# Performance work log

Measured on AMD Instinct MI355X. Metric: run time of the kernel, lower is better.

Reference implementation:

```python
import jax, jax.numpy as jnp
import numpy as np

N, D, H = 32768, 512, 8
HD = D // H  # head_dim = 64
LN_EPS = 1e-5


def setup_inputs() -> dict:
    key = jax.random.key(0)
    ks = jax.random.split(key, 5)
    s = 1.0 / np.sqrt(D)
    return {
        "h": jax.random.normal(ks[0], (N, D), dtype=jnp.float32),
        "Wq": jax.random.normal(ks[1], (D, D), dtype=jnp.float32) * s,
        "Wk": jax.random.normal(ks[2], (D, D), dtype=jnp.float32) * s,
        "Wv": jax.random.normal(ks[3], (D, D), dtype=jnp.float32) * s,
        "Wf": jax.random.normal(ks[4], (D, D), dtype=jnp.float32) * s,
        "ln_gamma": jnp.ones((D,), dtype=jnp.float32),
        "ln_beta": jnp.zeros((D,), dtype=jnp.float32),
    }


def _layernorm(x, g, b):
    mu = jnp.mean(x, axis=-1, keepdims=True)
    var = jnp.mean(jnp.square(x - mu), axis=-1, keepdims=True)
    return (x - mu) * jax.lax.rsqrt(var + LN_EPS) * g + b


def reference(h, Wq, Wk, Wv, Wf, ln_gamma, ln_beta):
    n = h.shape[0]
    # projections (torch Linear y = x @ W^T; weights here stored as [in,out])
    q = jax.nn.relu((h @ Wq).reshape(n, H, HD))
    k = jax.nn.relu((h @ Wk).reshape(n, H, HD))
    v = (h @ Wv).reshape(n, H, HD)
    # per-node outer-product accumulation over heads (n = head axis here)
    kv = jnp.einsum('bnd,bne->bde', k, v)          # [N, HD, HD]
    num = jnp.einsum('bnd,bde->bne', q, kv)        # [N, H, HD]
    denom = jnp.einsum('bnd,bd->bn', q, k.sum(axis=1))  # [N, H]
    attn = num / denom[..., None]                  # [N, H, HD]
    fh = attn.reshape(n, D) @ Wf                   # dropout = identity (eval)
    out = _layernorm(h + fh, ln_gamma, ln_beta)
    return (out, q, k, v)
```

## Files before the change

### kernel.cpp

```cpp
#include <hip/hip_runtime.h>
#include <hip/hip_bf16.h>

#define NROWS 32768
#define DIM   512
#define HEADS 8
#define LN_EPS 1e-5f

typedef __attribute__((ext_vector_type(8))) short short8;
typedef __attribute__((ext_vector_type(4))) float floatx4;

typedef __attribute__((address_space(3))) void lds_void;
typedef __attribute__((address_space(1))) void gbl_void;

__device__ __forceinline__ void async16(const void* g, void* l) {
    __builtin_amdgcn_global_load_lds(
        (gbl_void*)(unsigned long long)(uintptr_t)g,
        (lds_void*)(unsigned int)(uintptr_t)l,
        16, 0, 0);
}

__global__ __launch_bounds__(256) void hconv_kernel(
    const float* __restrict__ h, __hip_bfloat16* __restrict__ hb)
{
    const size_t i = ((size_t)blockIdx.x * 256 + threadIdx.x) * 4;
    const float4 f = *(const float4*)(h + i);
    union { ushort4 u; __hip_bfloat16 b[4]; } pk;
    pk.b[0] = __float2bfloat16(f.x);
    pk.b[1] = __float2bfloat16(f.y);
    pk.b[2] = __float2bfloat16(f.z);
    pk.b[3] = __float2bfloat16(f.w);
    *(ushort4*)(hb + i) = pk.u;
}

__global__ __launch_bounds__(256) void wtrans_kernel(
    const float* __restrict__ Wq, const float* __restrict__ Wk,
    const float* __restrict__ Wv, const float* __restrict__ Wf,
    __hip_bfloat16* __restrict__ Wt)
{
    __shared__ float tile[32][33];
    const int z = blockIdx.z;
    const float* W = (z == 0) ? Wq : (z == 1) ? Wk : (z == 2) ? Wv : Wf;
    __hip_bfloat16* dst = Wt + (size_t)z * DIM * DIM;

    const int bn = blockIdx.x * 32;
    const int bk = blockIdx.y * 32;
    const int tx = threadIdx.x & 31;
    const int ty = threadIdx.x >> 5;
    #pragma unroll
    for (int i = ty; i < 32; i += 8)
        tile[i][tx] = W[(size_t)(bk + i) * DIM + bn + tx];
    __syncthreads();
    #pragma unroll
    for (int i = ty; i < 32; i += 8)
        dst[(size_t)(bn + i) * DIM + bk + tx] = __float2bfloat16(tile[tx][i]);
}

__global__ __launch_bounds__(256) void mfma_gemm_kernel(
    const __hip_bfloat16* __restrict__ A,
    const __hip_bfloat16* __restrict__ Bt,
    float* __restrict__ C, int qkv)
{
    __shared__ __align__(16) char smem[32768];

    const int t    = threadIdx.x;
    const int lane = t & 63;
    const int w    = t >> 6;
    const int wm   = w >> 1, wn = w & 1;
    const int l16  = lane & 15, quad = lane >> 4;

    const int nwg  = gridDim.x * gridDim.y;
    int flat = blockIdx.y * gridDim.x + blockIdx.x;
    flat = (flat & 7) * (nwg >> 3) + (flat >> 3);
    const int bx = flat % gridDim.x;
    const int by = flat / gridDim.x;

    const int bm = by * 128;
    const int bn = bx * 128;

    float* Cp;
    int ccol, relu;
    if (qkv) {
        Cp   = C + (size_t)(bx >> 2) * ((size_t)NROWS * DIM);
        ccol = (bx & 3) * 128;
        relu = (bx >> 2) < 2;
    } else {
        Cp = C; ccol = bn; relu = 0;
    }

    const int c0 = w * 128 + lane;
    const int c1 = c0 + 64;
    const int r0 = c0 >> 2, kq0 = (c0 & 3) ^ ((r0 >> 1) & 3);
    const int r1 = c1 >> 2, kq1 = (c1 & 3) ^ ((r1 >> 1) & 3);

    const int offA0 = (bm + r0) * DIM + kq0 * 8;
    const int offA1 = (bm + r1) * DIM + kq1 * 8;
    const int offB0 = (bn + r0) * DIM + kq0 * 8;
    const int offB1 = (bn + r1) * DIM + kq1 * 8;
    const int ldsC0 = (w * 128) * 16;
    const int ldsC1 = (w * 128 + 64) * 16;

    int aoff[4], boff[4];
    #pragma unroll
    for (int i = 0; i < 4; ++i) {
        const int ra = wm * 64 + i * 16 + l16;
        aoff[i] = (ra * 4 + (quad ^ ((ra >> 1) & 3))) * 16;
        const int rb = wn * 64 + i * 16 + l16;
        boff[i] = 8192 + (rb * 4 + (quad ^ ((rb >> 1) & 3))) * 16;
    }

    floatx4 acc[4][4];
    #pragma unroll
    for (int i = 0; i < 4; ++i)
        #pragma unroll
        for (int j = 0; j < 4; ++j)
            acc[i][j] = (floatx4){0.f, 0.f, 0.f, 0.f};

    #define STAGE(tt) do {                                                  \
        char* _b = smem + ((tt) & 1) * 16384;                               \
        const int _k0 = (tt) * 32;                                          \
        async16(A  + offA0 + _k0, _b + ldsC0);                              \
        async16(A  + offA1 + _k0, _b + ldsC1);                              \
        async16(Bt + offB0 + _k0, _b + 8192 + ldsC0);                       \
        async16(Bt + offB1 + _k0, _b + 8192 + ldsC1);                       \
    } while (0)

    #define COMPUTE(tt) do {                                                \
        const char* _b = smem + ((tt) & 1) * 16384;                         \
        short8 af[4], bf[4];                                                \
        _Pragma("unroll")                                                   \
        for (int i = 0; i < 4; ++i) af[i] = *(const short8*)(_b + aoff[i]); \
        _Pragma("unroll")                                                   \
        for (int j = 0; j < 4; ++j) bf[j] = *(const short8*)(_b + boff[j]); \
        _Pragma("unroll")                                                   \
        for (int i = 0; i < 4; ++i)                                         \
            _Pragma("unroll")                                               \
            for (int j = 0; j < 4; ++j)                                     \
                acc[i][j] = __builtin_amdgcn_mfma_f32_16x16x32_bf16(        \
                    af[i], bf[j], acc[i][j], 0, 0, 0);                      \
    } while (0)

    STAGE(0);
    for (int kt = 0; kt < 15; ++kt) {
        STAGE(kt + 1);
        asm volatile("s_waitcnt vmcnt(4)\n\ts_barrier" ::: "memory");
        COMPUTE(kt);
        asm volatile("s_barrier" ::: "memory");
    }
    asm volatile("s_waitcnt vmcnt(0)\n\ts_barrier" ::: "memory");
    COMPUTE(15);

    #undef STAGE
    #undef COMPUTE

    #pragma unroll
    for (int i = 0; i < 4; ++i) {
        const int gr = bm + wm * 64 + i * 16 + quad * 4;
        #pragma unroll
        for (int j = 0; j < 4; ++j) {
            const int gc = ccol + wn * 64 + j * 16 + l16;
            #pragma unroll
            for (int rg = 0; rg < 4; ++rg) {
                float vv = acc[i][j][rg];
                if (relu) vv = fmaxf(vv, 0.f);
                Cp[(size_t)(gr + rg) * DIM + gc] = vv;
            }
        }
    }
}

__global__ __launch_bounds__(256) void attn_kernel(
    const float* __restrict__ q, const float* __restrict__ k,
    const float* __restrict__ v, __hip_bfloat16* __restrict__ attn)
{
    __shared__ float sq[4][8][68];
    __shared__ float sk[4][8][68];
    __shared__ float sv[4][8][68];

    const int t = threadIdx.x;
    const int w = t >> 6, lane = t & 63;
    const size_t base = ((size_t)blockIdx.x * 4 + w) * DIM;

    const int sh = lane >> 3;
    const int sd = (lane & 7) * 8;
    {
        const float4 q0 = ((const float4*)(q + base))[lane * 2];
        const float4 q1 = ((const float4*)(q + base))[lane * 2 + 1];
        const float4 k0 = ((const float4*)(k + base))[lane * 2];
        const float4 k1 = ((const float4*)(k + base))[lane * 2 + 1];
        const float4 v0 = ((const float4*)(v + base))[lane * 2];
        const float4 v1 = ((const float4*)(v + base))[lane * 2 + 1];
        *(float4*)&sq[w][sh][sd]     = q0;
        *(float4*)&sq[w][sh][sd + 4] = q1;
        *(float4*)&sk[w][sh][sd]     = k0;
        *(float4*)&sk[w][sh][sd + 4] = k1;
        *(float4*)&sv[w][sh][sd]     = v0;
        *(float4*)&sv[w][sh][sd + 4] = v1;
    }
    __syncthreads();

    const int n  = lane >> 3;
    const int hh = lane & 7;
    float s = 0.f;
    #pragma unroll
    for (int d = 0; d < 64; d += 4) {
        const float4 a = *(const float4*)&sq[w][n][d];
        const float4 b = *(const float4*)&sk[w][hh][d];
        s += a.x * b.x + a.y * b.y + a.z * b.z + a.w * b.w;
    }
    float den = s;
    den += __shfl_xor(den, 1);
    den += __shfl_xor(den, 2);
    den += __shfl_xor(den, 4);
    const float p = s / den;

    float pl[8];
    #pragma unroll
    for (int h = 0; h < 8; ++h) pl[h] = __shfl(p, (lane & 56) | h);

    const int eg = (lane & 7) * 8;
    float o[8] = {0.f, 0.f, 0.f, 0.f, 0.f, 0.f, 0.f, 0.f};
    #pragma unroll
    for (int h = 0; h < 8; ++h) {
        const float4 v0 = *(const float4*)&sv[w][h][eg];
        const float4 v1 = *(const float4*)&sv[w][h][eg + 4];
        o[0] += pl[h] * v0.x; o[1] += pl[h] * v0.y;
        o[2] += pl[h] * v0.z; o[3] += pl[h] * v0.w;
        o[4] += pl[h] * v1.x; o[5] += pl[h] * v1.y;
        o[6] += pl[h] * v1.z; o[7] += pl[h] * v1.w;
    }
    union { short8 s8; __hip_bfloat16 b[8]; } pk;
    #pragma unroll
    for (int j = 0; j < 8; ++j) pk.b[j] = __float2bfloat16(o[j]);
    *(short8*)(attn + base + (size_t)lane * 8) = pk.s8;
}

__global__ __launch_bounds__(256) void ln_kernel(
    const float* __restrict__ h, const float* fh,
    const float* __restrict__ gamma, const float* __restrict__ beta,
    float* out)
{
    const int lane = threadIdx.x & 63;
    const int wave = threadIdx.x >> 6;
    const size_t base = ((size_t)blockIdx.x * 4 + wave) * DIM;

    const float4 a0 = ((const float4*)(h + base))[lane * 2];
    const float4 a1 = ((const float4*)(h + base))[lane * 2 + 1];
    const float4 b0 = ((const float4*)(fh + base))[lane * 2];
    const float4 b1 = ((const float4*)(fh + base))[lane * 2 + 1];

    float x[8];
    x[0] = a0.x + b0.x; x[1] = a0.y + b0.y; x[2] = a0.z + b0.z; x[3] = a0.w + b0.w;
    x[4] = a1.x + b1.x; x[5] = a1.y + b1.y; x[6] = a1.z + b1.z; x[7] = a1.w + b1.w;

    float s = 0.f;
    #pragma unroll
    for (int i = 0; i < 8; ++i) s += x[i];
    #pragma unroll
    for (int off = 32; off > 0; off >>= 1) s += __shfl_down(s, off);
    const float mu = __shfl(s, 0) * (1.f / DIM);

    float vs = 0.f;
    #pragma unroll
    for (int i = 0; i < 8; ++i) { const float d = x[i] - mu; vs += d * d; }
    #pragma unroll
    for (int off = 32; off > 0; off >>= 1) vs += __shfl_down(vs, off);
    const float rstd = rsqrtf(__shfl(vs, 0) * (1.f / DIM) + LN_EPS);

    const float4 g0 = ((const float4*)gamma)[lane * 2];
    const float4 g1 = ((const float4*)gamma)[lane * 2 + 1];
    const float4 e0 = ((const float4*)beta)[lane * 2];
    const float4 e1 = ((const float4*)beta)[lane * 2 + 1];

    float4 r0, r1;
    r0.x = (x[0] - mu) * rstd * g0.x + e0.x;
    r0.y = (x[1] - mu) * rstd * g0.y + e0.y;
    r0.z = (x[2] - mu) * rstd * g0.z + e0.z;
    r0.w = (x[3] - mu) * rstd * g0.w + e0.w;
    r1.x = (x[4] - mu) * rstd * g1.x + e1.x;
    r1.y = (x[5] - mu) * rstd * g1.y + e1.y;
    r1.z = (x[6] - mu) * rstd * g1.z + e1.z;
    r1.w = (x[7] - mu) * rstd * g1.w + e1.w;

    ((float4*)(out + base))[lane * 2]     = r0;
    ((float4*)(out + base))[lane * 2 + 1] = r1;
}

extern "C" void kernel_launch(void* const* d_in, const int* in_sizes, int n_in,
                              void* d_out, int out_size, void* d_ws, size_t ws_size,
                              hipStream_t stream)
{
    const float* h     = (const float*)d_in[0];
    const float* Wq    = (const float*)d_in[1];
    const float* Wk    = (const float*)d_in[2];
    const float* Wv    = (const float*)d_in[3];
    const float* Wf    = (const float*)d_in[4];
    const float* gamma = (const float*)d_in[5];
    const float* beta  = (const float*)d_in[6];

    const size_t ND = (size_t)NROWS * DIM;
    float* out = (float*)d_out;
    float* qo  = out + ND;
    float* ko  = out + 2 * ND;
    float* vo  = out + 3 * ND;
    float* fh  = out;

    __hip_bfloat16* hb  = (__hip_bfloat16*)d_ws;
    __hip_bfloat16* wt  = hb + ND;
    __hip_bfloat16* wtf = wt + 3 * DIM * DIM;
    __hip_bfloat16* attnb = hb;

    hconv_kernel<<<NROWS * DIM / 1024, 256, 0, stream>>>(h, hb);
    wtrans_kernel<<<dim3(16, 16, 4), 256, 0, stream>>>(Wq, Wk, Wv, Wf, wt);

    mfma_gemm_kernel<<<dim3(12, NROWS / 128), 256, 0, stream>>>(hb, wt, qo, 1);

    attn_kernel<<<NROWS / 4, 256, 0, stream>>>(qo, ko, vo, attnb);

    mfma_gemm_kernel<<<dim3(4, NROWS / 128), 256, 0, stream>>>(attnb, wtf, fh, 0);

    ln_kernel<<<NROWS / 4, 256, 0, stream>>>(h, fh, gamma, beta, out);
}
```

Baseline: 442.3 us.

## Enlarge GEMM M-tile to 256 rows with 8x4 MFMA accumulators per wave

The bf16 MFMA GEMM block tile grows from 128x128 to 256x128. Each wave now computes 128x64 outputs with 32 accumulator tiles, and the LDS stages grow to 24 KB per buffer. The aim is better reuse of B tiles and a higher ratio of MFMA work to LDS reads, with half as many blocks. In exchange, register pressure roughly doubles (launch_bounds now asks for 2 blocks per CU), and the smaller grid may leave the machine less full, since these GEMMs are largely bound by the fp32 output stores.

```diff
diff --git a/kernel.cpp b/kernel.cpp
--- a/kernel.cpp
+++ b/kernel.cpp
@@ -55,12 +55,12 @@
         dst[(size_t)(bn + i) * DIM + bk + tx] = __float2bfloat16(tile[tx][i]);
 }
 
-__global__ __launch_bounds__(256) void mfma_gemm_kernel(
+__global__ __launch_bounds__(256, 2) void mfma_gemm_kernel(
     const __hip_bfloat16* __restrict__ A,
     const __hip_bfloat16* __restrict__ Bt,
     float* __restrict__ C, int qkv)
 {
-    __shared__ __align__(16) char smem[32768];
+    __shared__ __align__(16) char smem[49152];
 
     const int t    = threadIdx.x;
     const int lane = t & 63;
@@ -74,7 +74,7 @@
     const int bx = flat % gridDim.x;
     const int by = flat / gridDim.x;
 
-    const int bm = by * 128;
+    const int bm = by * 256;
     const int bn = bx * 128;
 
     float* Cp;
@@ -87,52 +87,62 @@
         Cp = C; ccol = bn; relu = 0;
     }
 
-    const int c0 = w * 128 + lane;
-    const int c1 = c0 + 64;
-    const int r0 = c0 >> 2, kq0 = (c0 & 3) ^ ((r0 >> 1) & 3);
-    const int r1 = c1 >> 2, kq1 = (c1 & 3) ^ ((r1 >> 1) & 3);
-
-    const int offA0 = (bm + r0) * DIM + kq0 * 8;
-    const int offA1 = (bm + r1) * DIM + kq1 * 8;
-    const int offB0 = (bn + r0) * DIM + kq0 * 8;
-    const int offB1 = (bn + r1) * DIM + kq1 * 8;
-    const int ldsC0 = (w * 128) * 16;
-    const int ldsC1 = (w * 128 + 64) * 16;
-
-    int aoff[4], boff[4];
-    #pragma unroll
-    for (int i = 0; i < 4; ++i) {
-        const int ra = wm * 64 + i * 16 + l16;
+    int offA[4], offB[2];
+    int ldsA[4], ldsB[2];
+    #pragma unroll
+    for (int s = 0; s < 4; ++s) {
+        const int p = w * 256 + s * 64 + lane;
+        const int r = p >> 2, kq = (p & 3) ^ ((r >> 1) & 3);
+        offA[s] = (bm + r) * DIM + kq * 8;
+        ldsA[s] = (w * 256 + s * 64) * 16;
+    }
+    #pragma unroll
+    for (int s = 0; s < 2; ++s) {
+        const int p = w * 128 + s * 64 + lane;
+        const int r = p >> 2, kq = (p & 3) ^ ((r >> 1) & 3);
+        offB[s] = (bn + r) * DIM + kq * 8;
+        ldsB[s] = 16384 + (w * 128 + s * 64) * 16;
+    }
+
+    int aoff[8], boff[4];
+    #pragma unroll
+    for (int i = 0; i < 8; ++i) {
+        const int ra = wm * 128 + i * 16 + l16;
         aoff[i] = (ra * 4 + (quad ^ ((ra >> 1) & 3))) * 16;
-        const int rb = wn * 64 + i * 16 + l16;
-        boff[i] = 8192 + (rb * 4 + (quad ^ ((rb >> 1) & 3))) * 16;
-    }
-
-    floatx4 acc[4][4];
-    #pragma unroll
-    for (int i = 0; i < 4; ++i)
+    }
+    #pragma unroll
+    for (int j = 0; j < 4; ++j) {
+        const int rb = wn * 64 + j * 16 + l16;
+        boff[j] = 16384 + (rb * 4 + (quad ^ ((rb >> 1) & 3))) * 16;
+    }
+
+    floatx4 acc[8][4];
+    #pragma unroll
+    for (int i = 0; i < 8; ++i)
         #pragma unroll
         for (int j = 0; j < 4; ++j)
             acc[i][j] = (floatx4){0.f, 0.f, 0.f, 0.f};
 
     #define STAGE(tt) do {                                                  \
-        char* _b = smem + ((tt) & 1) * 16384;                               \
+        char* _b = smem + ((tt) & 1) * 24576;                               \
         const int _k0 = (tt) * 32;                                          \
-        async16(A  + offA0 + _k0, _b + ldsC0);                              \
-        async16(A  + offA1 + _k0, _b + ldsC1);                              \
-        async16(Bt + offB0 + _k0, _b + 8192 + ldsC0);                       \
-        async16(Bt + offB1 + _k0, _b + 8192 + ldsC1);                       \
+        async16(A  + offA[0] + _k0, _b + ldsA[0]);                          \
+        async16(A  + offA[1] + _k0, _b + ldsA[1]);                          \
+        async16(A  + offA[2] + _k0, _b + ldsA[2]);                          \
+        async16(A  + offA[3] + _k0, _b + ldsA[3]);                          \
+        async16(Bt + offB[0] + _k0, _b + ldsB[0]);                          \
+        async16(Bt + offB[1] + _k0, _b + ldsB[1]);                          \
     } while (0)
 
     #define COMPUTE(tt) do {                                                \
-        const char* _b = smem + ((tt) & 1) * 16384;                         \
-        short8 af[4], bf[4];                                                \
+        const char* _b = smem + ((tt) & 1) * 24576;                         \
+        short8 af[8], bf[4];                                                \
         _Pragma("unroll")                                                   \
-        for (int i = 0; i < 4; ++i) af[i] = *(const short8*)(_b + aoff[i]); \
+        for (int i = 0; i < 8; ++i) af[i] = *(const short8*)(_b + aoff[i]); \
         _Pragma("unroll")                                                   \
         for (int j = 0; j < 4; ++j) bf[j] = *(const short8*)(_b + boff[j]); \
         _Pragma("unroll")                                                   \
-        for (int i = 0; i < 4; ++i)                                         \
+        for (int i = 0; i < 8; ++i)                                         \
             _Pragma("unroll")                                               \
             for (int j = 0; j < 4; ++j)                                     \
                 acc[i][j] = __builtin_amdgcn_mfma_f32_16x16x32_bf16(        \
@@ -142,7 +152,7 @@
     STAGE(0);
     for (int kt = 0; kt < 15; ++kt) {
         STAGE(kt + 1);
-        asm volatile("s_waitcnt vmcnt(4)\n\ts_barrier" ::: "memory");
+        asm volatile("s_waitcnt vmcnt(6)\n\ts_barrier" ::: "memory");
         COMPUTE(kt);
         asm volatile("s_barrier" ::: "memory");
     }
@@ -153,8 +163,8 @@
     #undef COMPUTE
 
     #pragma unroll
-    for (int i = 0; i < 4; ++i) {
-        const int gr = bm + wm * 64 + i * 16 + quad * 4;
+    for (int i = 0; i < 8; ++i) {
+        const int gr = bm + wm * 128 + i * 16 + quad * 4;
         #pragma unroll
         for (int j = 0; j < 4; ++j) {
             const int gc = ccol + wn * 64 + j * 16 + l16;
@@ -312,11 +322,11 @@
     hconv_kernel<<<NROWS * DIM / 1024, 256, 0, stream>>>(h, hb);
     wtrans_kernel<<<dim3(16, 16, 4), 256, 0, stream>>>(Wq, Wk, Wv, Wf, wt);
 
-    mfma_gemm_kernel<<<dim3(12, NROWS / 128), 256, 0, stream>>>(hb, wt, qo, 1);
+    mfma_gemm_kernel<<<dim3(12, NROWS / 256), 256, 0, stream>>>(hb, wt, qo, 1);
 
     attn_kernel<<<NROWS / 4, 256, 0, stream>>>(qo, ko, vo, attnb);
 
-    mfma_gemm_kernel<<<dim3(4, NROWS / 128), 256, 0, stream>>>(attnb, wtf, fh, 0);
+    mfma_gemm_kernel<<<dim3(4, NROWS / 256), 256, 0, stream>>>(attnb, wtf, fh, 0);
 
     ln_kernel<<<NROWS / 4, 256, 0, stream>>>(h, fh, gamma, beta, out);
 }
```

After: 440.8 us. About the same (-0.3%).
